# Performance work log

Measured on AMD Instinct MI355X. Metric: run time of the kernel, lower is better.

Reference implementation:

```python
import jax, jax.numpy as jnp
import numpy as np

B, C, I, H, T = 256, 16, 64, 40, 512


def setup_inputs() -> dict:
    key = jax.random.key(0)
    ks = jax.random.split(key, 7)
    s = 1.0 / np.sqrt(H)  # PyTorch GRU/Linear init scale
    return {
        "x": jax.random.normal(ks[0], (B, C, I, T), jnp.float32),
        "W_ih": jax.random.uniform(ks[1], (C, 3 * H, I), jnp.float32, -s, s),
        "W_hh": jax.random.uniform(ks[2], (C, 3 * H, H), jnp.float32, -s, s),
        "b_ih": jax.random.uniform(ks[3], (C, 3 * H), jnp.float32, -s, s),
        "b_hh": jax.random.uniform(ks[4], (C, 3 * H), jnp.float32, -s, s),
        "W_fc": jax.random.uniform(ks[5], (C, 1, H), jnp.float32, -s, s),
        "b_fc": jax.random.uniform(ks[6], (C, 1), jnp.float32, -s, s),
    }


def reference(x, W_ih, W_hh, b_ih, b_hh, W_fc, b_fc):
    # x: [B, C, I, T] -> time-major [T, B, C, I] (module permutes to batch_first [B,T,I] per channel)
    xt = jnp.transpose(x, (3, 0, 1, 2))
    hid = W_hh.shape[-1]
    # Precompute input projections for all steps/channels at once: [T, B, C, 3H]
    gi = jnp.einsum('tbci,cgi->tbcg', xt, W_ih) + b_ih

    def step(h, gi_t):
        # h: [B, C, H]
        gh = jnp.einsum('bch,cgh->bcg', h, W_hh) + b_hh  # [B, C, 3H]
        i_r, i_z, i_n = jnp.split(gi_t, 3, axis=-1)
        h_r, h_z, h_n = jnp.split(gh, 3, axis=-1)
        r = jax.nn.sigmoid(i_r + h_r)
        z = jax.nn.sigmoid(i_z + h_z)
        n = jnp.tanh(i_n + r * h_n)
        h_new = (1.0 - z) * n + z * h
        return h_new, None

    h0 = jnp.zeros((x.shape[0], x.shape[1], hid), x.dtype)
    h_final, _ = jax.lax.scan(step, h0, gi)  # final hidden [B, C, H]

    # Channel-wise FC (H -> 1) + sigmoid: [B, C, 1]
    y = jnp.einsum('bch,coh->bco', h_final, W_fc) + b_fc
    return jax.nn.sigmoid(y)
```

## Files before the change

kernel.cpp:

```cpp
#include <hip/hip_runtime.h>

#define B_ 256
#define C_ 16
#define I_ 64
#define H_ 40
#define T_ 512
#define G_ 120

#define TT  16
#define NCH (T_ / TT)
#define NT  640

#define SX  72
#define SHB 72

typedef short bf16x8 __attribute__((ext_vector_type(8)));
typedef float f32x4  __attribute__((ext_vector_type(4)));

__device__ __forceinline__ unsigned short f2bf(float f) {
    unsigned u = __float_as_uint(f);
    unsigned r = (u + 0x7FFFu + ((u >> 16) & 1u)) >> 16;
    return (unsigned short)r;
}
__device__ __forceinline__ float bf2f(unsigned s) {
    return __uint_as_float(s << 16);
}
__device__ __forceinline__ float sigf(float x) {
    return __builtin_amdgcn_rcpf(1.0f + __expf(-x));
}

__global__ __launch_bounds__(NT, 1)
void gru_mfma_kernel(const float* __restrict__ x,
                     const float* __restrict__ Wih,
                     const float* __restrict__ Whh,
                     const float* __restrict__ bih,
                     const float* __restrict__ bhh,
                     const float* __restrict__ Wfc,
                     const float* __restrict__ bfc,
                     float* __restrict__ out)
{
    __shared__ __align__(16) unsigned short xa[256 * SX];
    __shared__ __align__(16) unsigned short hbf[2][16 * SHB];

    const int tid = threadIdx.x;
    const int c   = blockIdx.x >> 4;
    const int b0  = (blockIdx.x & 15) * 16;
    const int w   = tid >> 6;
    const int lan = tid & 63;
    const int lq  = lan >> 4;
    const int lm  = lan & 15;
    const int k   = w * 4 + lq;

    for (int idx = tid; idx < 2 * 16 * SHB; idx += NT)
        ((unsigned short*)hbf)[idx] = 0;

    float hreg = 0.0f;

    float4 pf[7];
#define PREFETCH(T0)                                                           \
    {                                                                          \
        _Pragma("unroll")                                                      \
        for (int it = 0; it < 7; ++it) {                                       \
            int idx = tid + it * NT;                                           \
            if (idx < 4096) {                                                  \
                int q = idx & 3, i = (idx >> 2) & 63, b = idx >> 8;            \
                const float* p = x + ((((size_t)(b0 + b) * C_ + c) * I_ + i)   \
                                      * T_ + (T0) + q * 4);                    \
                pf[it] = *reinterpret_cast<const float4*>(p);                  \
            }                                                                  \
        }                                                                      \
    }

    PREFETCH(0);

    bf16x8 wihf[2], whhf[2];
    {
        const int p  = w * 16 + lm;
        const int pg = p & 3;
        const int pk = p >> 2;
        #pragma unroll
        for (int ks = 0; ks < 2; ++ks) {
            bf16x8 a  = {0,0,0,0,0,0,0,0};
            bf16x8 hh = {0,0,0,0,0,0,0,0};
            if (pg < 3) {
                const float* wp = Wih + ((size_t)c * G_ + pg * H_ + pk) * I_ + ks * 32 + lq * 8;
                float4 v0 = *reinterpret_cast<const float4*>(wp);
                float4 v1 = *reinterpret_cast<const float4*>(wp + 4);
                a[0]=(short)f2bf(v0.x); a[1]=(short)f2bf(v0.y);
                a[2]=(short)f2bf(v0.z); a[3]=(short)f2bf(v0.w);
                a[4]=(short)f2bf(v1.x); a[5]=(short)f2bf(v1.y);
                a[6]=(short)f2bf(v1.z); a[7]=(short)f2bf(v1.w);
                if (ks == 0 || lq == 0) {
                    const float* hp = Whh + ((size_t)c * G_ + pg * H_ + pk) * H_ + ks * 32 + lq * 8;
                    float4 u0 = *reinterpret_cast<const float4*>(hp);
                    float4 u1 = *reinterpret_cast<const float4*>(hp + 4);
                    hh[0]=(short)f2bf(u0.x); hh[1]=(short)f2bf(u0.y);
                    hh[2]=(short)f2bf(u0.z); hh[3]=(short)f2bf(u0.w);
                    hh[4]=(short)f2bf(u1.x); hh[5]=(short)f2bf(u1.y);
                    hh[6]=(short)f2bf(u1.z); hh[7]=(short)f2bf(u1.w);
                }
            }
            wihf[ks] = a;
            whhf[ks] = hh;
        }
    }

    f32x4 bias4;
    #pragma unroll
    for (int r = 0; r < 4; ++r) {
        float v = 0.0f;
        if (r < 3) v  = bhh[c * G_ + r * H_ + k];
        if (r < 2) v += bih[c * G_ + r * H_ + k];
        bias4[r] = v;
    }
    const float bihn = bih[c * G_ + 2 * H_ + k];
    const float wfck = Wfc[c * H_ + k];

    uint2 gi_reg[16];

    for (int ch = 0; ch < NCH; ++ch) {
        #pragma unroll
        for (int it = 0; it < 7; ++it) {
            int idx = tid + it * NT;
            if (idx < 4096) {
                int q = idx & 3, i = (idx >> 2) & 63, b = idx >> 8;
                int colp = (((i >> 3) ^ q) << 3) | (i & 7);
                float4 v = pf[it];
                unsigned short* xr = &xa[(q * 64 + b) * SX + colp];
                xr[0]       = f2bf(v.x);
                xr[16 * SX] = f2bf(v.y);
                xr[32 * SX] = f2bf(v.z);
                xr[48 * SX] = f2bf(v.w);
            }
        }
        __syncthreads();

        { int tn = (ch + 1 < NCH) ? (ch + 1) * TT : 0; PREFETCH(tn); }

        #pragma unroll
        for (int nt = 0; nt < 16; ++nt) {
            const unsigned short* xp = &xa[(nt * 16 + lm) * SX + ((lq ^ (nt >> 2)) << 3)];
            bf16x8 xb0 = *reinterpret_cast<const bf16x8*>(xp);
            bf16x8 xb1 = *reinterpret_cast<const bf16x8*>(xp + 32);
            f32x4 acc = {0.f, 0.f, 0.f, 0.f};
            acc = __builtin_amdgcn_mfma_f32_16x16x32_bf16(wihf[0], xb0, acc, 0, 0, 0);
            acc = __builtin_amdgcn_mfma_f32_16x16x32_bf16(wihf[1], xb1, acc, 0, 0, 0);
            gi_reg[nt].x = (unsigned)f2bf(acc[0]) | ((unsigned)f2bf(acc[1]) << 16);
            gi_reg[nt].y = (unsigned)f2bf(acc[2]) | ((unsigned)f2bf(acc[3]) << 16);
        }

        #pragma unroll
        for (int tt = 0; tt < TT; ++tt) {
            const unsigned short* hp = &hbf[tt & 1][lm * SHB + lq * 8];
            bf16x8 h0 = *reinterpret_cast<const bf16x8*>(hp);
            bf16x8 h1 = {0,0,0,0,0,0,0,0};
            if (lq == 0)
                h1 = *reinterpret_cast<const bf16x8*>(&hbf[tt & 1][lm * SHB + 32]);
            f32x4 a1 = bias4;
            a1 = __builtin_amdgcn_mfma_f32_16x16x32_bf16(whhf[0], h0, a1, 0, 0, 0);
            f32x4 a2 = {0.f, 0.f, 0.f, 0.f};
            a2 = __builtin_amdgcn_mfma_f32_16x16x32_bf16(whhf[1], h1, a2, 0, 0, 0);
            uint2 gv = gi_reg[tt];
            float pre_r = a1[0] + a2[0] + bf2f(gv.x & 0xffffu);
            float pre_z = a1[1] + a2[1] + bf2f(gv.x >> 16);
            float h_n   = a1[2] + a2[2];
            float i_n   = bf2f(gv.y & 0xffffu) + bihn;
            float r = sigf(pre_r);
            float z = sigf(pre_z);
            float e = __expf(2.0f * (i_n + r * h_n));
            float n = 1.0f - 2.0f * __builtin_amdgcn_rcpf(e + 1.0f);
            hreg = (1.0f - z) * n + z * hreg;
            hbf[(tt & 1) ^ 1][lm * SHB + k] = f2bf(hreg);
            __syncthreads();
        }
    }

    float* red = reinterpret_cast<float*>(xa);
    red[tid] = hreg * wfck;
    __syncthreads();
    if (tid < 16) {
        float s = bfc[c];
        #pragma unroll
        for (int kk = 0; kk < H_; ++kk) s += red[kk * 16 + tid];
        out[(b0 + tid) * C_ + c] = sigf(s);
    }
}

extern "C" void kernel_launch(void* const* d_in, const int* in_sizes, int n_in,
                              void* d_out, int out_size, void* d_ws, size_t ws_size,
                              hipStream_t stream) {
    const float* x   = (const float*)d_in[0];
    const float* Wih = (const float*)d_in[1];
    const float* Whh = (const float*)d_in[2];
    const float* bih = (const float*)d_in[3];
    const float* bhh = (const float*)d_in[4];
    const float* Wfc = (const float*)d_in[5];
    const float* bfc = (const float*)d_in[6];
    float* out = (float*)d_out;

    dim3 grid(C_ * (B_ / 16));
    dim3 block(NT);
    gru_mfma_kernel<<<grid, block, 0, stream>>>(x, Wih, Whh, bih, bhh, Wfc, bfc, out);
}
```

Measured before the change: 803.9 us.

## Double-buffer x tile and interleave input projection with recurrent steps

Doubles the shared x staging buffer so the next chunk's bf16 staging and the global prefetch happen inside the recurrent step loop instead of in a separate phase with a block-wide barrier. The input-projection MFMAs are spread across the time steps, two steps ahead, so their latency can overlap the serial recurrence. It also replaces __syncthreads with a lighter barrier that waits only on LDS counters, leaving global prefetch loads outstanding across steps. Risks include higher register pressure, more LDS use, and subtle ordering hazards from the weaker barrier.

Measured after the change: 810.0 us. No clear change (+0.7%).

```diff
diff --git a/kernel.cpp b/kernel.cpp
--- a/kernel.cpp
+++ b/kernel.cpp
@@ -27,6 +27,12 @@
 }
 __device__ __forceinline__ float sigf(float x) {
     return __builtin_amdgcn_rcpf(1.0f + __expf(-x));
+}
+
+__device__ __forceinline__ void step_barrier() {
+    asm volatile("s_waitcnt lgkmcnt(0)" ::: "memory");
+    __builtin_amdgcn_s_barrier();
+    asm volatile("" ::: "memory");
 }
 
 __global__ __launch_bounds__(NT, 1)
@@ -39,7 +45,7 @@
                      const float* __restrict__ bfc,
                      float* __restrict__ out)
 {
-    __shared__ __align__(16) unsigned short xa[256 * SX];
+    __shared__ __align__(16) unsigned short xa[2][256 * SX];
     __shared__ __align__(16) unsigned short hbf[2][16 * SHB];
 
     const int tid = threadIdx.x;
@@ -67,6 +73,24 @@
                 const float* p = x + ((((size_t)(b0 + b) * C_ + c) * I_ + i)   \
                                       * T_ + (T0) + q * 4);                    \
                 pf[it] = *reinterpret_cast<const float4*>(p);                  \
+            }                                                                  \
+        }                                                                      \
+    }
+
+#define STAGE(bufi)                                                            \
+    {                                                                          \
+        _Pragma("unroll")                                                      \
+        for (int it = 0; it < 7; ++it) {                                       \
+            int idx = tid + it * NT;                                           \
+            if (idx < 4096) {                                                  \
+                int q = idx & 3, i = (idx >> 2) & 63, b = idx >> 8;            \
+                int colp = (((i >> 3) ^ q) << 3) | (i & 7);                    \
+                float4 v = pf[it];                                             \
+                unsigned short* xr = &xa[bufi][(q * 64 + b) * SX + colp];      \
+                xr[0]       = f2bf(v.x);                                       \
+                xr[16 * SX] = f2bf(v.y);                                       \
+                xr[32 * SX] = f2bf(v.z);                                       \
+                xr[48 * SX] = f2bf(v.w);                                       \
             }                                                                  \
         }                                                                      \
     }
@@ -118,39 +142,35 @@
 
     uint2 gi_reg[16];
 
+#define GI(bufi, nt)                                                             \
+    {                                                                            \
+        const unsigned short* xp =                                               \
+            &xa[bufi][((nt) * 16 + lm) * SX + ((lq ^ ((nt) >> 2)) << 3)];        \
+        bf16x8 xb0 = *reinterpret_cast<const bf16x8*>(xp);                       \
+        bf16x8 xb1 = *reinterpret_cast<const bf16x8*>(xp + 32);                  \
+        f32x4 acc = {0.f, 0.f, 0.f, 0.f};                                        \
+        acc = __builtin_amdgcn_mfma_f32_16x16x32_bf16(wihf[0], xb0, acc, 0, 0, 0);\
+        acc = __builtin_amdgcn_mfma_f32_16x16x32_bf16(wihf[1], xb1, acc, 0, 0, 0);\
+        gi_reg[nt].x = (unsigned)f2bf(acc[0]) | ((unsigned)f2bf(acc[1]) << 16);  \
+        gi_reg[nt].y = (unsigned)f2bf(acc[2]) | ((unsigned)f2bf(acc[3]) << 16);  \
+    }
+
+    STAGE(0);
+    step_barrier();
+    PREFETCH(TT);
+
     for (int ch = 0; ch < NCH; ++ch) {
-        #pragma unroll
-        for (int it = 0; it < 7; ++it) {
-            int idx = tid + it * NT;
-            if (idx < 4096) {
-                int q = idx & 3, i = (idx >> 2) & 63, b = idx >> 8;
-                int colp = (((i >> 3) ^ q) << 3) | (i & 7);
-                float4 v = pf[it];
-                unsigned short* xr = &xa[(q * 64 + b) * SX + colp];
-                xr[0]       = f2bf(v.x);
-                xr[16 * SX] = f2bf(v.y);
-                xr[32 * SX] = f2bf(v.z);
-                xr[48 * SX] = f2bf(v.w);
-            }
-        }
-        __syncthreads();
-
-        { int tn = (ch + 1 < NCH) ? (ch + 1) * TT : 0; PREFETCH(tn); }
-
-        #pragma unroll
-        for (int nt = 0; nt < 16; ++nt) {
-            const unsigned short* xp = &xa[(nt * 16 + lm) * SX + ((lq ^ (nt >> 2)) << 3)];
-            bf16x8 xb0 = *reinterpret_cast<const bf16x8*>(xp);
-            bf16x8 xb1 = *reinterpret_cast<const bf16x8*>(xp + 32);
-            f32x4 acc = {0.f, 0.f, 0.f, 0.f};
-            acc = __builtin_amdgcn_mfma_f32_16x16x32_bf16(wihf[0], xb0, acc, 0, 0, 0);
-            acc = __builtin_amdgcn_mfma_f32_16x16x32_bf16(wihf[1], xb1, acc, 0, 0, 0);
-            gi_reg[nt].x = (unsigned)f2bf(acc[0]) | ((unsigned)f2bf(acc[1]) << 16);
-            gi_reg[nt].y = (unsigned)f2bf(acc[2]) | ((unsigned)f2bf(acc[3]) << 16);
-        }
+        const int cur = ch & 1;
+
+        GI(cur, 0);
+        GI(cur, 1);
 
         #pragma unroll
         for (int tt = 0; tt < TT; ++tt) {
+            if (tt + 2 < TT) GI(cur, tt + 2);
+            if (tt == 10 && ch + 1 < NCH) STAGE(cur ^ 1);
+            if (tt == 11 && ch + 2 < NCH) PREFETCH((ch + 2) * TT);
+
             const unsigned short* hp = &hbf[tt & 1][lm * SHB + lq * 8];
             bf16x8 h0 = *reinterpret_cast<const bf16x8*>(hp);
             bf16x8 h1 = {0,0,0,0,0,0,0,0};
@@ -171,11 +191,11 @@
             float n = 1.0f - 2.0f * __builtin_amdgcn_rcpf(e + 1.0f);
             hreg = (1.0f - z) * n + z * hreg;
             hbf[(tt & 1) ^ 1][lm * SHB + k] = f2bf(hreg);
-            __syncthreads();
+            step_barrier();
         }
     }
 
-    float* red = reinterpret_cast<float*>(xa);
+    float* red = reinterpret_cast<float*>(&xa[0][0]);
     red[tid] = hreg * wfck;
     __syncthreads();
     if (tid < 16) {
```
